# Optimization experiments

Measured on AMD Instinct MI355X. Metric: run time of the kernel, lower is better.

The kernel has to match this reference:

```python
import jax, jax.numpy as jnp
import numpy as np

L = 5   # num GIN layers
D = 128 # input_dim == hidden_dim
BN_EPS = 1e-5

def _bn(x, g, b):
    # training-mode BatchNorm1d over nodes: biased variance, eps=1e-5
    m = jnp.mean(x, axis=0)
    v = jnp.var(x, axis=0)
    return g * (x - m) * jax.lax.rsqrt(v + BN_EPS) + b

def setup_inputs() -> dict:
    key = jax.random.key(0)
    ks = jax.random.split(key, 12)
    N, E = 50000, 800000
    h = jax.random.normal(ks[0], (N, D), dtype=jnp.float32)
    src = jax.random.randint(ks[1], (E,), 0, N)
    dst = jax.random.randint(ks[2], (E,), 0, N)
    s = 1.0 / np.sqrt(D)
    W1 = jax.random.uniform(ks[3], (L, D, D), jnp.float32, -s, s)
    b1 = jax.random.uniform(ks[4], (L, D), jnp.float32, -s, s)
    W2 = jax.random.uniform(ks[5], (L, D, D), jnp.float32, -s, s)
    b2 = jax.random.uniform(ks[6], (L, D), jnp.float32, -s, s)
    bn1_g = jax.random.uniform(ks[7], (L, D), jnp.float32, 0.5, 1.5)
    bn1_b = jax.random.normal(ks[8], (L, D), jnp.float32) * 0.1
    bn2_g = jax.random.uniform(ks[9], (L, D), jnp.float32, 0.5, 1.5)
    bn2_b = jax.random.normal(ks[10], (L, D), jnp.float32) * 0.1
    bn3_g = jax.random.uniform(ks[11], (L, D), jnp.float32, 0.5, 1.5)
    bn3_b = jnp.zeros((L, D), jnp.float32)
    return dict(h=h, src=src, dst=dst, W1=W1, b1=b1, W2=W2, b2=b2,
                bn1_g=bn1_g, bn1_b=bn1_b, bn2_g=bn2_g, bn2_b=bn2_b,
                bn3_g=bn3_g, bn3_b=bn3_b)

def reference(h, src, dst, W1, b1, W2, b2, bn1_g, bn1_b, bn2_g, bn2_b, bn3_g, bn3_b):
    N = h.shape[0]
    for l in range(L):
        # GINConv, sum aggregation, eps = 0: (1+eps)*h + sum_{j->i} h_j
        agg = jax.ops.segment_sum(h[src], dst, num_segments=N)
        rst = h + agg
        # MLP: linear -> BN -> ReLU -> linear (linear output)
        x = rst @ W1[l] + b1[l]
        x = jax.nn.relu(_bn(x, bn1_g[l], bn1_b[l]))
        x = x @ W2[l] + b2[l]
        # ApplyNodeFunc: BN + ReLU
        x = jax.nn.relu(_bn(x, bn2_g[l], bn2_b[l]))
        # GIN outer BatchNorm + ReLU
        h = jax.nn.relu(_bn(x, bn3_g[l], bn3_b[l]))
    return h
```

## Files before the change

kernel.cpp:

```cpp
#include <hip/hip_runtime.h>
#include <hip/hip_bf16.h>
#include <cstdint>

#define BN_EPS 1e-5f
#define CSR_SHIFT 7
#define NBMAX 512

typedef __attribute__((ext_vector_type(8))) short short8;
typedef __attribute__((ext_vector_type(8))) __bf16 bf16x8;
typedef __attribute__((ext_vector_type(4))) float f32x4;

__device__ inline short f2bf(float f) {
    union { float f; unsigned u; } v; v.f = f;
    unsigned r = v.u + 0x7fffu + ((v.u >> 16) & 1u);
    return (short)(r >> 16);
}
__device__ inline float bf2f(short h) {
    union { unsigned u; float f; } v;
    v.u = ((unsigned)(unsigned short)h) << 16;
    return v.f;
}
__device__ inline unsigned asu(float f) { union { float f; unsigned u; } v; v.f = f; return v.u; }
__device__ inline float asf(unsigned u) { union { unsigned u; float f; } v; v.u = u; return v.f; }


__global__ __launch_bounds__(256) void setup_kernel(
    const float* __restrict__ h, unsigned short* __restrict__ hb, int total4,
    const float* __restrict__ W1, const float* __restrict__ W2,
    short* __restrict__ WtHi, short* __restrict__ WtLo,
    float* __restrict__ stats, int nstats, int* __restrict__ bcnt, int nb) {
    int i = blockIdx.x * 256 + threadIdx.x;
    if (i < nstats) stats[i] = 0.f;
    if (i < nb) bcnt[i] = 0;
    if (i < 10 * 128 * 128) {
        int mat = i >> 14, n = (i >> 7) & 127, k = i & 127;
        const float* W = (mat < 5) ? (W1 + mat * 16384) : (W2 + (mat - 5) * 16384);
        float w = W[k * 128 + n];
        short hi = f2bf(w);
        WtHi[i] = hi;
        WtLo[i] = f2bf(w - bf2f(hi));
    }
    if (i < total4) {
        float4 v = ((const float4*)h)[i];
        ushort4 o;
        o.x = (unsigned short)f2bf(v.x);
        o.y = (unsigned short)f2bf(v.y);
        o.z = (unsigned short)f2bf(v.z);
        o.w = (unsigned short)f2bf(v.w);
        ((ushort4*)hb)[i] = o;
    }
}


__global__ __launch_bounds__(256) void bcount_kernel(const int* __restrict__ dst,
                                                     int* __restrict__ bucketCnt,
                                                     int E, int nb, int chunk) {
    __shared__ int hist[NBMAX];
    int t = threadIdx.x;
    for (int i = t; i < nb; i += 256) hist[i] = 0;
    __syncthreads();
    int s = blockIdx.x * chunk, e = s + chunk; if (e > E) e = E;
    for (int i = s + t; i < e; i += 256) atomicAdd(&hist[dst[i] >> CSR_SHIFT], 1);
    __syncthreads();
    for (int i = t; i < nb; i += 256) if (hist[i]) atomicAdd(&bucketCnt[i], hist[i]);
}

__global__ __launch_bounds__(512) void bscan_kernel(const int* __restrict__ bucketCnt,
                                                    int* __restrict__ bucketBase,
                                                    int* __restrict__ bucketCursor,
                                                    int* __restrict__ rowptr,
                                                    int nb, int N, int E) {
    __shared__ int ps[NBMAX];
    int t = threadIdx.x;
    int v = (t < nb) ? bucketCnt[t] : 0;
    ps[t] = v;
    __syncthreads();
#pragma unroll
    for (int off = 1; off < NBMAX; off <<= 1) {
        int u = 0;
        if (t >= off) u = ps[t - off];
        __syncthreads();
        ps[t] += u;
        __syncthreads();
    }
    if (t < nb) {
        int b = ps[t] - v;
        bucketBase[t] = b;
        bucketCursor[t] = b;
    }
    if (t == 0) { bucketBase[nb] = E; rowptr[N] = E; }
}

__global__ __launch_bounds__(256) void bscatter_kernel(const int* __restrict__ src,
                                                       const int* __restrict__ dst,
                                                       int* __restrict__ bucketCursor,
                                                       uint2* __restrict__ pairs,
                                                       int E, int nb, int chunk) {
    __shared__ int cnt[NBMAX];
    __shared__ int base[NBMAX];
    int t = threadIdx.x;
    for (int i = t; i < nb; i += 256) cnt[i] = 0;
    __syncthreads();
    int s = blockIdx.x * chunk, e = s + chunk; if (e > E) e = E;
    for (int i = s + t; i < e; i += 256) atomicAdd(&cnt[dst[i] >> CSR_SHIFT], 1);
    __syncthreads();
    for (int i = t; i < nb; i += 256) {
        int c = cnt[i];
        base[i] = c ? atomicAdd(&bucketCursor[i], c) : 0;
    }
    __syncthreads();
    for (int i = t; i < nb; i += 256) cnt[i] = 0;
    __syncthreads();
    for (int i = s + t; i < e; i += 256) {
        int d = dst[i];
        int b = d >> CSR_SHIFT;
        int slot = atomicAdd(&cnt[b], 1);
        pairs[base[b] + slot] = make_uint2((unsigned)src[i], (unsigned)d);
    }
}

__global__ __launch_bounds__(256) void bbuild_kernel(const uint2* __restrict__ pairs,
                                                     const int* __restrict__ bucketBase,
                                                     int* __restrict__ rowptr,
                                                     int* __restrict__ colidx, int N) {
    __shared__ int cnt[128];
    int b = blockIdx.x, t = threadIdx.x;
    int lo = bucketBase[b], hi = bucketBase[b + 1];
    if (t < 128) cnt[t] = 0;
    __syncthreads();
    for (int e = lo + t; e < hi; e += 256) atomicAdd(&cnt[pairs[e].y & 127], 1);
    __syncthreads();
    int orig = (t < 128) ? cnt[t] : 0;
#pragma unroll
    for (int o = 1; o < 128; o <<= 1) {
        int u = 0;
        if (t < 128 && t >= o) u = cnt[t - o];
        __syncthreads();
        if (t < 128) cnt[t] += u;
        __syncthreads();
    }
    int ex = (t < 128) ? (cnt[t] - orig) : 0;
    if (t < 128) {
        int node = b * 128 + t;
        if (node < N) rowptr[node] = lo + ex;
    }
    __syncthreads();
    if (t < 128) cnt[t] = ex;
    __syncthreads();
    for (int e = lo + t; e < hi; e += 256) {
        uint2 p = pairs[e];
        int slot = atomicAdd(&cnt[p.y & 127], 1);
        colidx[lo + slot] = (int)p.x * 64;
    }
}

__device__ inline void coeff_from_stats(const float* __restrict__ stats,
                                        const float* __restrict__ g,
                                        const float* __restrict__ bb,
                                        int col, int N, float& a, float& c) {
    float s = 0.f, q = 0.f;
#pragma unroll
    for (int st = 0; st < 8; ++st) {
        s += stats[st * 256 + col];
        q += stats[st * 256 + 128 + col];
    }
    float m = s / N, v = q / N - m * m;
    a = g[col] * rsqrtf(v + BN_EPS);
    c = bb[col] - m * a;
}

__device__ inline void folded_coeffs(
    const float* __restrict__ stats2, const float* __restrict__ g2, const float* __restrict__ b2v,
    const float* __restrict__ stats3, const float* __restrict__ g3, const float* __restrict__ b3v,
    int col, int N, float& A, float& C, float& D) {
    float a2, c2, a3, c3;
    coeff_from_stats(stats2, g2, b2v, col, N, a2, c2);
    coeff_from_stats(stats3, g3, b3v, col, N, a3, c3);
    A = a3 * a2;
    C = fmaf(a3, c2, c3);
    D = fmaxf(c3, 0.f);
}


template <int MODE>
__global__ __launch_bounds__(256) void agg_kernel(
    const unsigned short* __restrict__ Xb, const int* __restrict__ rowptr,
    const int* __restrict__ colidx,
    const float* __restrict__ stats2, const float* __restrict__ g2, const float* __restrict__ b2v,
    const float* __restrict__ stats3, const float* __restrict__ g3, const float* __restrict__ b3v,
    float* __restrict__ rst, int N) {
    __shared__ float cf[3][128];
    int t = threadIdx.x;
    if (MODE) {
        if (t < 128) {
            float A, C, D;
            folded_coeffs(stats2, g2, b2v, stats3, g3, b3v, t, N, A, C, D);
            cf[0][t] = A; cf[1][t] = C; cf[2][t] = D;
        }
        __syncthreads();
    }
    int wv = __builtin_amdgcn_readfirstlane(t >> 6);
    int node = blockIdx.x * 4 + wv;
    if (node >= N) return;
    int lane = t & 63;
    int c0 = lane * 2, c1 = c0 + 1;
    float A0 = 1.f, C0 = 0.f, D0 = 0.f, A1 = 1.f, C1 = 0.f, D1 = 0.f;
    if (MODE) {
        A0 = cf[0][c0]; A1 = cf[0][c1];
        C0 = cf[1][c0]; C1 = cf[1][c1];
        D0 = cf[2][c0]; D1 = cf[2][c1];
    }
    auto fx = [&](float u) { return MODE ? fmaxf(fmaf(A0, u, C0), D0) : u; };
    auto fy = [&](float u) { return MODE ? fmaxf(fmaf(A1, u, C1), D1) : u; };
    const ushort2* X2 = (const ushort2*)Xb;
    ushort2 self = X2[node * 64 + lane];
    float ax = fx(bf2f((short)self.x)), ay = fy(bf2f((short)self.y));
    int e = rowptr[node], end = rowptr[node + 1];
    for (; e + 16 <= end; e += 16) {
        int j[16];
#pragma unroll
        for (int k = 0; k < 16; ++k) j[k] = colidx[e + k];
        ushort2 v[16];
#pragma unroll
        for (int k = 0; k < 16; ++k) v[k] = X2[j[k] + lane];
#pragma unroll
        for (int k = 0; k < 16; ++k) {
            ax += fx(bf2f((short)v[k].x));
            ay += fy(bf2f((short)v[k].y));
        }
    }
    for (; e + 4 <= end; e += 4) {
        int j[4];
#pragma unroll
        for (int k = 0; k < 4; ++k) j[k] = colidx[e + k];
        ushort2 v[4];
#pragma unroll
        for (int k = 0; k < 4; ++k) v[k] = X2[j[k] + lane];
#pragma unroll
        for (int k = 0; k < 4; ++k) {
            ax += fx(bf2f((short)v[k].x));
            ay += fy(bf2f((short)v[k].y));
        }
    }
    for (; e < end; ++e) {
        ushort2 v = X2[colidx[e] + lane];
        ax += fx(bf2f((short)v.x));
        ay += fy(bf2f((short)v.y));
    }
    float2 r; r.x = ax; r.y = ay;
    ((float2*)rst)[node * 64 + lane] = r;
}


template <int PRE, int OUTBF>
__global__ __launch_bounds__(256, 2) void gemm_kernel(
    const float* __restrict__ A,
    const short* __restrict__ WtHi, const short* __restrict__ WtLo,
    const float* __restrict__ bias,
    const float* __restrict__ preStats, const float* __restrict__ preG,
    const float* __restrict__ preB,
    float* __restrict__ C, unsigned short* __restrict__ Cb,
    float* __restrict__ outStats, int N) {
    __shared__ short WsHi[128 * 128];
    __shared__ short WsLo[128 * 128];

    const int t = threadIdx.x;
    const int row0 = blockIdx.x * 128;
    const int w = t >> 6, lane = t & 63;
    const int quad = lane >> 4, l16 = lane & 15;
    const int sw = (l16 & 7) * 8;

    float aE = 1.f, cE = 0.f, aO = 1.f, cO = 0.f;
    if (PRE) {
        coeff_from_stats(preStats, preG, preB, lane * 2, N, aE, cE);
        coeff_from_stats(preStats, preG, preB, lane * 2 + 1, N, aO, cO);
    }

    float4 af[2][4][2];
#pragma unroll
    for (int m = 0; m < 2; ++m) {
        int gr = row0 + w * 32 + m * 16 + l16;
        bool ok = gr < N;
        const float* Ar = A + (size_t)gr * 128;
#pragma unroll
        for (int kk = 0; kk < 4; ++kk) {
            int kb = kk * 32 + quad * 8;
            af[m][kk][0] = ok ? *(const float4*)(Ar + kb) : make_float4(0.f, 0.f, 0.f, 0.f);
            af[m][kk][1] = ok ? *(const float4*)(Ar + kb + 4) : make_float4(0.f, 0.f, 0.f, 0.f);
        }
    }

#pragma unroll
    for (int i = 0; i < 8; ++i) {
        int ch = t + i * 256;
        int r = ch >> 4, k = (ch & 15) * 8;
        int d = r * 128 + (k ^ ((r & 7) * 8));
        *(short8*)(WsHi + d) = *(const short8*)(WtHi + r * 128 + k);
        *(short8*)(WsLo + d) = *(const short8*)(WtLo + r * 128 + k);
    }
    __syncthreads();

    short8 fh[2][4], fl[2][4];
#pragma unroll
    for (int kk = 0; kk < 4; ++kk) {
        float a8[8], c8[8];
#pragma unroll
        for (int j = 0; j < 8; ++j) {
            if (PRE) {
                int col = kk * 32 + quad * 8 + j;
                int srcl = col >> 1;
                a8[j] = __shfl((j & 1) ? aO : aE, srcl, 64);
                c8[j] = __shfl((j & 1) ? cO : cE, srcl, 64);
            }
        }
#pragma unroll
        for (int m = 0; m < 2; ++m) {
            float x[8];
            *(float4*)(x) = af[m][kk][0];
            *(float4*)(x + 4) = af[m][kk][1];
            short8 h, lo;
#pragma unroll
            for (int j = 0; j < 4; ++j) {
                float x0 = x[2 * j], x1 = x[2 * j + 1];
                if (PRE) {
                    x0 = fmaxf(a8[2 * j] * x0 + c8[2 * j], 0.f);
                    x1 = fmaxf(a8[2 * j + 1] * x1 + c8[2 * j + 1], 0.f);
                }
                unsigned u0 = asu(x0), u1 = asu(x1);
                unsigned hp = __builtin_amdgcn_perm(u1, u0, 0x07060302u);
                float l0 = x0 - asf(u0 & 0xFFFF0000u);
                float l1 = x1 - asf(u1 & 0xFFFF0000u);
                unsigned lp = __builtin_amdgcn_perm(asu(l1), asu(l0), 0x07060302u);
                ((unsigned*)&h)[j] = hp;
                ((unsigned*)&lo)[j] = lp;
            }
            fh[m][kk] = h;
            fl[m][kk] = lo;
        }
    }

    f32x4 acc[2][8];
#pragma unroll
    for (int m = 0; m < 2; ++m)
#pragma unroll
        for (int n = 0; n < 8; ++n) acc[m][n] = (f32x4){0.f, 0.f, 0.f, 0.f};

#pragma unroll
    for (int kk = 0; kk < 4; ++kk) {
        int kb = kk * 32 + quad * 8;
        bf16x8 a0h = __builtin_bit_cast(bf16x8, fh[0][kk]);
        bf16x8 a1h = __builtin_bit_cast(bf16x8, fh[1][kk]);
        bf16x8 a0l = __builtin_bit_cast(bf16x8, fl[0][kk]);
        bf16x8 a1l = __builtin_bit_cast(bf16x8, fl[1][kk]);
#pragma unroll
        for (int n = 0; n < 8; ++n) {
            int woff = (n * 16 + l16) * 128 + (kb ^ sw);
            bf16x8 bh = __builtin_bit_cast(bf16x8, *(const short8*)(WsHi + woff));
            bf16x8 bl = __builtin_bit_cast(bf16x8, *(const short8*)(WsLo + woff));
            acc[0][n] = __builtin_amdgcn_mfma_f32_16x16x32_bf16(a0h, bh, acc[0][n], 0, 0, 0);
            acc[0][n] = __builtin_amdgcn_mfma_f32_16x16x32_bf16(a0l, bh, acc[0][n], 0, 0, 0);
            acc[0][n] = __builtin_amdgcn_mfma_f32_16x16x32_bf16(a0h, bl, acc[0][n], 0, 0, 0);
            acc[1][n] = __builtin_amdgcn_mfma_f32_16x16x32_bf16(a1h, bh, acc[1][n], 0, 0, 0);
            acc[1][n] = __builtin_amdgcn_mfma_f32_16x16x32_bf16(a1l, bh, acc[1][n], 0, 0, 0);
            acc[1][n] = __builtin_amdgcn_mfma_f32_16x16x32_bf16(a1h, bl, acc[1][n], 0, 0, 0);
        }
    }

    __syncthreads();

    float bv[8];
#pragma unroll
    for (int n = 0; n < 8; ++n) bv[n] = bias[n * 16 + l16];
    float ls[8], lsq[8];
#pragma unroll
    for (int n = 0; n < 8; ++n) { ls[n] = 0.f; lsq[n] = 0.f; }
#pragma unroll
    for (int m = 0; m < 2; ++m) {
        int rbase = row0 + w * 32 + m * 16 + quad * 4;
#pragma unroll
        for (int n = 0; n < 8; ++n) {
#pragma unroll
            for (int r = 0; r < 4; ++r) {
                int row = rbase + r;
                if (row < N) {
                    float val = acc[m][n][r] + bv[n];
                    if (OUTBF) val = bf2f(f2bf(val));
                    acc[m][n][r] = val;
                    ls[n] += val;
                    lsq[n] += val * val;
                }
            }
        }
    }

    float* P = (float*)WsHi;
#pragma unroll
    for (int n = 0; n < 8; ++n) {
        float s = ls[n], q = lsq[n];
        s += __shfl_xor(s, 16, 64);
        s += __shfl_xor(s, 32, 64);
        q += __shfl_xor(q, 16, 64);
        q += __shfl_xor(q, 32, 64);
        if (quad == 0) {
            int colv = n * 16 + l16;
            P[w * 512 + colv] = s;
            P[w * 512 + 256 + colv] = q;
        }
    }
    __syncthreads();

    int stripe = blockIdx.x & 7;
    if (t < 128) {
        int col = t;
        float S = P[col] + P[512 + col] + P[1024 + col] + P[1536 + col];
        atomicAdd(&outStats[stripe * 256 + col], S);
    } else {
        int col = t - 128;
        float Q = P[256 + col] + P[768 + col] + P[1280 + col] + P[1792 + col];
        atomicAdd(&outStats[stripe * 256 + 128 + col], Q);
    }

#pragma unroll
    for (int m = 0; m < 2; ++m) {
        int rbase = row0 + w * 32 + m * 16 + quad * 4;
#pragma unroll
        for (int n = 0; n < 8; ++n) {
            int colv = n * 16 + l16;
#pragma unroll
            for (int r = 0; r < 4; ++r) {
                int row = rbase + r;
                if (row < N) {
                    if (OUTBF)
                        Cb[(size_t)row * 128 + colv] = (unsigned short)f2bf(acc[m][n][r]);
                    else
                        C[(size_t)row * 128 + colv] = acc[m][n][r];
                }
            }
        }
    }
}


__global__ __launch_bounds__(256) void elt_kernel(
    const unsigned short* __restrict__ Xb,
    const float* __restrict__ inStats, const float* __restrict__ g, const float* __restrict__ bb,
    float* __restrict__ outStats, int N) {
    __shared__ float red[256 * 8];
    __shared__ float cf[2][128];
    int t = threadIdx.x;
    if (t < 128) {
        float a, c;
        coeff_from_stats(inStats, g, bb, t, N, a, c);
        cf[0][t] = a; cf[1][t] = c;
    }
    __syncthreads();
    int cg = t & 31;
    float a[4], c[4];
#pragma unroll
    for (int k = 0; k < 4; ++k) {
        a[k] = cf[0][cg * 4 + k];
        c[k] = cf[1][cg * 4 + k];
    }
    float sum[4] = {0.f, 0.f, 0.f, 0.f}, sq[4] = {0.f, 0.f, 0.f, 0.f};
    int total = N * 32;
    for (int i = blockIdx.x * 256 + t; i < total; i += gridDim.x * 256) {
        ushort4 u = ((const ushort4*)Xb)[i];
        float y0 = fmaxf(a[0] * bf2f((short)u.x) + c[0], 0.f);
        float y1 = fmaxf(a[1] * bf2f((short)u.y) + c[1], 0.f);
        float y2 = fmaxf(a[2] * bf2f((short)u.z) + c[2], 0.f);
        float y3 = fmaxf(a[3] * bf2f((short)u.w) + c[3], 0.f);
        sum[0] += y0; sq[0] += y0 * y0;
        sum[1] += y1; sq[1] += y1 * y1;
        sum[2] += y2; sq[2] += y2 * y2;
        sum[3] += y3; sq[3] += y3 * y3;
    }
#pragma unroll
    for (int k = 0; k < 4; ++k) { red[t * 8 + k] = sum[k]; red[t * 8 + 4 + k] = sq[k]; }
    __syncthreads();
    if (t < 32) {
        float S[4] = {0.f, 0.f, 0.f, 0.f}, Q[4] = {0.f, 0.f, 0.f, 0.f};
        for (int j = 0; j < 8; ++j) {
            int tt = t + 32 * j;
#pragma unroll
            for (int k = 0; k < 4; ++k) { S[k] += red[tt * 8 + k]; Q[k] += red[tt * 8 + 4 + k]; }
        }
        int stripe = blockIdx.x & 7;
#pragma unroll
        for (int k = 0; k < 4; ++k) {
            atomicAdd(&outStats[stripe * 256 + t * 4 + k], S[k]);
            atomicAdd(&outStats[stripe * 256 + 128 + t * 4 + k], Q[k]);
        }
    }
}


__global__ __launch_bounds__(256) void final_kernel(
    const unsigned short* __restrict__ Xb,
    const float* __restrict__ stats2, const float* __restrict__ g2, const float* __restrict__ b2v,
    const float* __restrict__ stats3, const float* __restrict__ g3, const float* __restrict__ b3v,
    float* __restrict__ out, int N) {
    __shared__ float cf[3][128];
    int t = threadIdx.x;
    if (t < 128) {
        float A, C, D;
        folded_coeffs(stats2, g2, b2v, stats3, g3, b3v, t, N, A, C, D);
        cf[0][t] = A; cf[1][t] = C; cf[2][t] = D;
    }
    __syncthreads();
    int cg = t & 31;
    float A[4], C[4], D[4];
#pragma unroll
    for (int k = 0; k < 4; ++k) {
        int colv = cg * 4 + k;
        A[k] = cf[0][colv];
        C[k] = cf[1][colv];
        D[k] = cf[2][colv];
    }
    int total = N * 32;
    for (int i = blockIdx.x * 256 + t; i < total; i += gridDim.x * 256) {
        ushort4 u = ((const ushort4*)Xb)[i];
        float4 y;
        y.x = fmaxf(fmaf(A[0], bf2f((short)u.x), C[0]), D[0]);
        y.y = fmaxf(fmaf(A[1], bf2f((short)u.y), C[1]), D[1]);
        y.z = fmaxf(fmaf(A[2], bf2f((short)u.z), C[2]), D[2]);
        y.w = fmaxf(fmaf(A[3], bf2f((short)u.w), C[3]), D[3]);
        ((float4*)out)[i] = y;
    }
}


extern "C" void kernel_launch(void* const* d_in, const int* in_sizes, int n_in,
                              void* d_out, int out_size, void* d_ws, size_t ws_size,
                              hipStream_t stream) {
    const float* h0   = (const float*)d_in[0];
    const int*   src  = (const int*)d_in[1];
    const int*   dst  = (const int*)d_in[2];
    const float* W1   = (const float*)d_in[3];
    const float* b1   = (const float*)d_in[4];
    const float* W2   = (const float*)d_in[5];
    const float* b2   = (const float*)d_in[6];
    const float* bn1g = (const float*)d_in[7];
    const float* bn1b = (const float*)d_in[8];
    const float* bn2g = (const float*)d_in[9];
    const float* bn2b = (const float*)d_in[10];
    const float* bn3g = (const float*)d_in[11];
    const float* bn3b = (const float*)d_in[12];
    const int N = in_sizes[0] / 128;
    const int E = in_sizes[1];
    const int nb = (N + 127) >> CSR_SHIFT;

    char* ws = (char*)d_ws;
    size_t off = 0;
    auto alloc = [&](size_t bytes) {
        void* p = ws + off;
        off = (off + bytes + 255) & ~(size_t)255;
        return p;
    };
    float* stats        = (float*)alloc((size_t)5 * 3 * 8 * 256 * sizeof(float));
    int*   bucketCnt    = (int*)alloc((size_t)NBMAX * 4);
    int*   bucketBase   = (int*)alloc((size_t)(NBMAX + 1) * 4);
    int*   bucketCursor = (int*)alloc((size_t)NBMAX * 4);
    int*   rowptr       = (int*)alloc((size_t)(N + 1) * 4);
    int*   colidx       = (int*)alloc((size_t)E * 4);
    uint2* pairs        = (uint2*)alloc((size_t)E * 8);
    short* WtHi         = (short*)alloc((size_t)10 * 16384 * 2);
    short* WtLo         = (short*)alloc((size_t)10 * 16384 * 2);
    float* buf0         = (float*)alloc((size_t)N * 128 * 4);
    float* buf1         = (float*)alloc((size_t)N * 128 * 4);
    unsigned short* xbf = (unsigned short*)alloc((size_t)N * 128 * 2);

    auto statsBase = [&](int l, int which) { return stats + ((size_t)(l * 3 + which)) * 8 * 256; };

    const int nstats = 5 * 3 * 8 * 256;
    int total4 = N * 32;
    setup_kernel<<<(total4 + 255) / 256, 256, 0, stream>>>(
        h0, xbf, total4, W1, W2, WtHi, WtLo, stats, nstats, bucketCnt, nb);

    const int chunk = 4096;
    const int chunkGrid = (E + chunk - 1) / chunk;
    bcount_kernel<<<chunkGrid, 256, 0, stream>>>(dst, bucketCnt, E, nb, chunk);
    bscan_kernel<<<1, 512, 0, stream>>>(bucketCnt, bucketBase, bucketCursor, rowptr, nb, N, E);
    bscatter_kernel<<<chunkGrid, 256, 0, stream>>>(src, dst, bucketCursor, pairs, E, nb, chunk);
    bbuild_kernel<<<nb, 256, 0, stream>>>(pairs, bucketBase, rowptr, colidx, N);

    const int gemmGrid = (N + 127) / 128;
    const int aggGrid = (N + 3) / 4;
    for (int l = 0; l < 5; ++l) {
        if (l == 0) {
            agg_kernel<0><<<aggGrid, 256, 0, stream>>>(
                xbf, rowptr, colidx,
                nullptr, nullptr, nullptr, nullptr, nullptr, nullptr,
                buf0, N);
        } else {
            int lp = l - 1;
            agg_kernel<1><<<aggGrid, 256, 0, stream>>>(
                xbf, rowptr, colidx,
                statsBase(lp, 1), bn2g + lp * 128, bn2b + lp * 128,
                statsBase(lp, 2), bn3g + lp * 128, bn3b + lp * 128,
                buf0, N);
        }
        gemm_kernel<0, 0><<<gemmGrid, 256, 0, stream>>>(
            buf0, WtHi + l * 16384, WtLo + l * 16384, b1 + l * 128,
            nullptr, nullptr, nullptr,
            buf1, nullptr, statsBase(l, 0), N);
        gemm_kernel<1, 1><<<gemmGrid, 256, 0, stream>>>(
            buf1, WtHi + (5 + l) * 16384, WtLo + (5 + l) * 16384, b2 + l * 128,
            statsBase(l, 0), bn1g + l * 128, bn1b + l * 128,
            nullptr, xbf, statsBase(l, 1), N);
        elt_kernel<<<256, 256, 0, stream>>>(
            xbf, statsBase(l, 1), bn2g + l * 128, bn2b + l * 128,
            statsBase(l, 2), N);
    }
    final_kernel<<<512, 256, 0, stream>>>(
        xbf,
        statsBase(4, 1), bn2g + 4 * 128, bn2b + 4 * 128,
        statsBase(4, 2), bn3g + 4 * 128, bn3b + 4 * 128,
        (float*)d_out, N);
}
```

Measured before the change: 535.3 us.

## Drop LDS weight staging in GEMM, read weights from global, raise occupancy

The GEMM kernel stops copying the split hi/lo bf16 weight matrices into 64 KB of shared memory and reads the MFMA B fragments straight from global memory (L1/L2 cached). BN pre-coefficients now go through a small shared table instead of wave shuffles, and outputs are stored inside the stats loop. Launch bounds rise to 3 blocks per SM. This removes the per-block weight staging and barrier and frees LDS for more resident blocks, at the cost of repeated global/L2 weight loads in the inner MFMA loop and possibly more register pressure.

```diff
diff --git a/kernel.cpp b/kernel.cpp
--- a/kernel.cpp
+++ b/kernel.cpp
@@ -253,7 +253,7 @@
 
 
 template <int PRE, int OUTBF>
-__global__ __launch_bounds__(256, 2) void gemm_kernel(
+__global__ __launch_bounds__(256, 3) void gemm_kernel(
     const float* __restrict__ A,
     const short* __restrict__ WtHi, const short* __restrict__ WtLo,
     const float* __restrict__ bias,
@@ -261,20 +261,13 @@
     const float* __restrict__ preB,
     float* __restrict__ C, unsigned short* __restrict__ Cb,
     float* __restrict__ outStats, int N) {
-    __shared__ short WsHi[128 * 128];
-    __shared__ short WsLo[128 * 128];
+    __shared__ float P[2048];
+    __shared__ float cf[2][128];
 
     const int t = threadIdx.x;
     const int row0 = blockIdx.x * 128;
     const int w = t >> 6, lane = t & 63;
     const int quad = lane >> 4, l16 = lane & 15;
-    const int sw = (l16 & 7) * 8;
-
-    float aE = 1.f, cE = 0.f, aO = 1.f, cO = 0.f;
-    if (PRE) {
-        coeff_from_stats(preStats, preG, preB, lane * 2, N, aE, cE);
-        coeff_from_stats(preStats, preG, preB, lane * 2 + 1, N, aO, cO);
-    }
 
     float4 af[2][4][2];
 #pragma unroll
@@ -290,28 +283,25 @@
         }
     }
 
-#pragma unroll
-    for (int i = 0; i < 8; ++i) {
-        int ch = t + i * 256;
-        int r = ch >> 4, k = (ch & 15) * 8;
-        int d = r * 128 + (k ^ ((r & 7) * 8));
-        *(short8*)(WsHi + d) = *(const short8*)(WtHi + r * 128 + k);
-        *(short8*)(WsLo + d) = *(const short8*)(WtLo + r * 128 + k);
-    }
-    __syncthreads();
+    if (PRE) {
+        if (t < 128) {
+            float a, c;
+            coeff_from_stats(preStats, preG, preB, t, N, a, c);
+            cf[0][t] = a; cf[1][t] = c;
+        }
+        __syncthreads();
+    }
 
     short8 fh[2][4], fl[2][4];
 #pragma unroll
     for (int kk = 0; kk < 4; ++kk) {
         float a8[8], c8[8];
-#pragma unroll
-        for (int j = 0; j < 8; ++j) {
-            if (PRE) {
-                int col = kk * 32 + quad * 8 + j;
-                int srcl = col >> 1;
-                a8[j] = __shfl((j & 1) ? aO : aE, srcl, 64);
-                c8[j] = __shfl((j & 1) ? cO : cE, srcl, 64);
-            }
+        if (PRE) {
+            int colb = kk * 32 + quad * 8;
+            *(float4*)(a8)     = *(const float4*)(&cf[0][colb]);
+            *(float4*)(a8 + 4) = *(const float4*)(&cf[0][colb + 4]);
+            *(float4*)(c8)     = *(const float4*)(&cf[1][colb]);
+            *(float4*)(c8 + 4) = *(const float4*)(&cf[1][colb + 4]);
         }
 #pragma unroll
         for (int m = 0; m < 2; ++m) {
@@ -354,9 +344,9 @@
         bf16x8 a1l = __builtin_bit_cast(bf16x8, fl[1][kk]);
 #pragma unroll
         for (int n = 0; n < 8; ++n) {
-            int woff = (n * 16 + l16) * 128 + (kb ^ sw);
-            bf16x8 bh = __builtin_bit_cast(bf16x8, *(const short8*)(WsHi + woff));
-            bf16x8 bl = __builtin_bit_cast(bf16x8, *(const short8*)(WsLo + woff));
+            int woff = (n * 16 + l16) * 128 + kb;
+            bf16x8 bh = __builtin_bit_cast(bf16x8, *(const short8*)(WtHi + woff));
+            bf16x8 bl = __builtin_bit_cast(bf16x8, *(const short8*)(WtLo + woff));
             acc[0][n] = __builtin_amdgcn_mfma_f32_16x16x32_bf16(a0h, bh, acc[0][n], 0, 0, 0);
             acc[0][n] = __builtin_amdgcn_mfma_f32_16x16x32_bf16(a0l, bh, acc[0][n], 0, 0, 0);
             acc[0][n] = __builtin_amdgcn_mfma_f32_16x16x32_bf16(a0h, bl, acc[0][n], 0, 0, 0);
@@ -366,8 +356,6 @@
         }
     }
 
-    __syncthreads();
-
     float bv[8];
 #pragma unroll
     for (int n = 0; n < 8; ++n) bv[n] = bias[n * 16 + l16];
@@ -379,21 +367,28 @@
         int rbase = row0 + w * 32 + m * 16 + quad * 4;
 #pragma unroll
         for (int n = 0; n < 8; ++n) {
+            int colv = n * 16 + l16;
 #pragma unroll
             for (int r = 0; r < 4; ++r) {
                 int row = rbase + r;
                 if (row < N) {
                     float val = acc[m][n][r] + bv[n];
-                    if (OUTBF) val = bf2f(f2bf(val));
-                    acc[m][n][r] = val;
-                    ls[n] += val;
-                    lsq[n] += val * val;
+                    if (OUTBF) {
+                        short hb = f2bf(val);
+                        float vr = bf2f(hb);
+                        Cb[(size_t)row * 128 + colv] = (unsigned short)hb;
+                        ls[n] += vr;
+                        lsq[n] += vr * vr;
+                    } else {
+                        C[(size_t)row * 128 + colv] = val;
+                        ls[n] += val;
+                        lsq[n] += val * val;
+                    }
                 }
             }
         }
     }
 
-    float* P = (float*)WsHi;
 #pragma unroll
     for (int n = 0; n < 8; ++n) {
         float s = ls[n], q = lsq[n];
@@ -418,25 +413,6 @@
         int col = t - 128;
         float Q = P[256 + col] + P[768 + col] + P[1280 + col] + P[1792 + col];
         atomicAdd(&outStats[stripe * 256 + 128 + col], Q);
-    }
-
-#pragma unroll
-    for (int m = 0; m < 2; ++m) {
-        int rbase = row0 + w * 32 + m * 16 + quad * 4;
-#pragma unroll
-        for (int n = 0; n < 8; ++n) {
-            int colv = n * 16 + l16;
-#pragma unroll
-            for (int r = 0; r < 4; ++r) {
-                int row = rbase + r;
-                if (row < N) {
-                    if (OUTBF)
-                        Cb[(size_t)row * 128 + colv] = (unsigned short)f2bf(acc[m][n][r]);
-                    else
-                        C[(size_t)row * 128 + colv] = acc[m][n][r];
-                }
-            }
-        }
     }
 }
 
```

New measurement: 637.0 us. 19.0% more time.
